# Performance work log

Measured on AMD Instinct MI355X. Metric: run time of the kernel, lower is better.

## Reference

```python
import jax, jax.numpy as jnp
import numpy as np

WS = 800      # window size
HEADS = 3
DH = 24       # dim_head
LOWRANK_W = 30
NEG_SLOPE = 0.01  # LeakyReLU default
LN_EPS = 1e-5


def _layernorm(x, g, b):
    m = jnp.mean(x, axis=-1, keepdims=True)
    v = jnp.var(x, axis=-1, keepdims=True)
    return (x - m) * jax.lax.rsqrt(v + LN_EPS) * g + b


def setup_inputs() -> dict:
    key = jax.random.key(0)
    ks = jax.random.split(key, 20)
    B, CIN, H, W = 2, 5, 160, 160
    D = 48
    INNER = HEADS * DH  # 72
    f32 = jnp.float32

    def n(k, shape, s=0.05):
        return jax.random.normal(k, shape, f32) * s

    return {
        "x": jax.random.normal(ks[0], (B, CIN, H, W), f32),
        # Embedding: Conv2d(5, 48, 3, pad=1) + PReLU
        "conv_w": n(ks[1], (D, CIN, 3, 3), 0.1),
        "conv_b": jnp.zeros((D,), f32),
        "prelu_a": jnp.array(0.25, f32),
        # attention PreNorm
        "ln1_g": jnp.ones((D,), f32),
        "ln1_b": jnp.zeros((D,), f32),
        # to_qkv: Linear(48, 216, bias=False)
        "w_qkv": n(ks[2], (3 * INNER, D)),
        # Linformer low-rank params E,F: [heads, dim_head, w]
        "E_mat": jax.random.normal(ks[3], (HEADS, DH, LOWRANK_W), f32),
        "F_mat": jax.random.normal(ks[4], (HEADS, DH, LOWRANK_W), f32),
        # lin1/lin2: Linear(w, dim_head)
        "w_e": n(ks[5], (DH, LOWRANK_W)),
        "b_e": jnp.zeros((DH,), f32),
        "w_f": n(ks[6], (DH, LOWRANK_W)),
        "b_f": jnp.zeros((DH,), f32),
        # to_out: Linear(72, 48)
        "w_out": n(ks[7], (D, INNER)),
        "b_out": jnp.zeros((D,), f32),
        # FF PreNorm + MLP (dim=48, hidden=48)
        "ln2_g": jnp.ones((D,), f32),
        "ln2_b": jnp.zeros((D,), f32),
        "ff_w1": n(ks[8], (D, D)),
        "ff_b1": jnp.zeros((D,), f32),
        "ff_w2": n(ks[9], (D, D)),
        "ff_b2": jnp.zeros((D,), f32),
        # final lin1: Linear(48, 96)
        "w_fin": n(ks[10], (2 * D, D)),
        "b_fin": jnp.zeros((2 * D,), f32),
    }


def reference(x, conv_w, conv_b, prelu_a, ln1_g, ln1_b, w_qkv, E_mat, F_mat,
              w_e, b_e, w_f, b_f, w_out, b_out, ln2_g, ln2_b,
              ff_w1, ff_b1, ff_w2, ff_b2, w_fin, b_fin):
    B, _, H, W = x.shape
    # Embedding: conv3x3 same + PReLU
    E = jax.lax.conv_general_dilated(
        x, conv_w, (1, 1), ((1, 1), (1, 1)),
        dimension_numbers=("NCHW", "OIHW", "NCHW")) + conv_b[None, :, None, None]
    E = jnp.maximum(E, 0) + prelu_a * jnp.minimum(E, 0)
    D = E.shape[1]
    seq = E.reshape(B, D, H * W).transpose(0, 2, 1)  # [B, N, D]
    N = seq.shape[1]
    nw = N // WS

    # --- Residual(PreNorm(LinformerAttention_wind1)) ---
    xn = _layernorm(seq, ln1_g, ln1_b)
    xw = xn.reshape(B, nw, WS, D)                         # windows
    qkv = jnp.einsum("bwnc,oc->bwno", xw, w_qkv)          # [B,nw,WS,216]
    qkv = qkv.reshape(B, nw, WS, HEADS, 3 * DH).transpose(0, 1, 3, 2, 4)
    q, k, v = jnp.split(qkv, 3, axis=-1)                  # each [B,nw,h,WS,DH]
    # einsum 'b h n d, h d d -> b h n d' == scale by diagonal of lin(E/F)
    e_diag = jnp.einsum("hdw,dw->hd", E_mat, w_e) + b_e   # [h, DH]
    f_diag = jnp.einsum("hdw,dw->hd", F_mat, w_f) + b_f
    k = k * e_diag[None, None, :, None, :]
    v = v * f_diag[None, None, :, None, :]
    scale = DH ** -0.5
    dots = jnp.einsum("bwhid,bwhjd->bwhij", q, k) * scale  # [B,nw,h,WS,WS]
    attn = jax.nn.softmax(dots, axis=-1)
    ow = jnp.einsum("bwhij,bwhjd->bwhid", attn, v)
    ow = ow.transpose(0, 1, 3, 2, 4).reshape(B, N, HEADS * DH)
    att = jnp.einsum("bnf,of->bno", ow, w_out) + b_out
    seq = seq + att

    # --- Residual(PreNorm(FeedForward)) ---
    yn = _layernorm(seq, ln2_g, ln2_b)
    h = jnp.einsum("bnc,oc->bno", yn, ff_w1) + ff_b1
    h = jnp.where(h >= 0, h, NEG_SLOPE * h)
    h = jnp.einsum("bno,co->bnc", h, ff_w2) + ff_b2
    att1 = seq + h                                        # [B, N, D]

    hp = att1.transpose(0, 2, 1).reshape(B, D, H, W)
    Highpass1 = E * hp + E
    lin = jnp.einsum("bnc,oc->bno", att1, w_fin) + b_fin  # [B, N, 2D]
    return (Highpass1, lin)
```

## Files before the change

kernel.cpp:

```cpp
#include <hip/hip_runtime.h>
#include <hip/hip_bf16.h>

#define B_    2
#define CIN_  5
#define H_    160
#define W_    160
#define N_    25600
#define D_    48
#define NW_   32
#define WS_   800
#define HEADS_ 3
#define DH_   24
#define INNER_ 72
#define NWH_  192

typedef __bf16 bf16x8 __attribute__((ext_vector_type(8)));
typedef float  f32x4  __attribute__((ext_vector_type(4)));

#define MFMA(a,b,c) __builtin_amdgcn_mfma_f32_16x16x32_bf16((a),(b),(c),0,0,0)

__device__ __forceinline__ float fast_exp2(float x) {
#if __has_builtin(__builtin_amdgcn_exp2f)
    return __builtin_amdgcn_exp2f(x);
#else
    return exp2f(x);
#endif
}

__device__ __forceinline__ unsigned pack_bf16(float lo, float hi) {
    __bf16 l = (__bf16)lo, h = (__bf16)hi;
    unsigned short ul = __builtin_bit_cast(unsigned short, l);
    unsigned short uh = __builtin_bit_cast(unsigned short, h);
    return ((unsigned)uh << 16) | (unsigned)ul;
}

__global__ __launch_bounds__(256) void k_wprep(const float* __restrict__ wqkv,
                                               const float* __restrict__ w_out,
                                               const float* __restrict__ fw1,
                                               const float* __restrict__ fw2,
                                               const float* __restrict__ wfin,
                                               const float* __restrict__ cw,
                                               const float* __restrict__ Em,
                                               const float* __restrict__ Fm,
                                               const float* __restrict__ we,
                                               const float* __restrict__ be,
                                               const float* __restrict__ wf,
                                               const float* __restrict__ bf,
                                               float* __restrict__ diag,
                                               __bf16* __restrict__ wqB,
                                               __bf16* __restrict__ woB,
                                               __bf16* __restrict__ f1B,
                                               __bf16* __restrict__ f2B,
                                               __bf16* __restrict__ wfB,
                                               __bf16* __restrict__ wcB) {
    if (blockIdx.x == 0 && threadIdx.x < 72) {
        int tt = threadIdx.x;
        int h = tt / 24, d = tt % 24;
        float se = be[d], sf = bf[d];
        for (int w = 0; w < 30; ++w) {
            se += Em[(h*24+d)*30 + w] * we[d*30 + w];
            sf += Fm[(h*24+d)*30 + w] * wf[d*30 + w];
        }
        diag[tt]      = se;
        diag[72 + tt] = sf;
    }
    int t = blockIdx.x*256 + threadIdx.x, stride = gridDim.x*256;
    for (int i = t; i < 288*64; i += stride) {
        int grow = i>>6, c = i&63;
        int gg = grow>>5, q = grow&31, tt = q>>4, sp = q&15, d = tt*16+sp;
        int part = gg/3, head = gg%3;
        wqB[i] = (d<24 && c<48) ? (__bf16)wqkv[(head*72 + part*24 + d)*48 + c] : (__bf16)0.f;
    }
    for (int i = t; i < 48*96;  i += stride) {
        int o = i/96, p = i%96;
        int h = p>>5, q = p&31, j = q&1, sp = q>>1, d = j*16+sp;
        woB[i] = (d<24) ? (__bf16)w_out[o*72 + h*24 + d] : (__bf16)0.f;
    }
    for (int i = t; i < 48*64;  i += stride) { int o=i>>6, c=i&63; f1B[i] = (c<48)? (__bf16)fw1[o*48+c] : (__bf16)0.f; }
    for (int i = t; i < 48*64;  i += stride) { int o=i>>6, c=i&63; f2B[i] = (c<48)? (__bf16)fw2[o*48+c] : (__bf16)0.f; }
    for (int i = t; i < 96*64;  i += stride) { int o=i>>6, c=i&63; wfB[i] = (c<48)? (__bf16)wfin[o*48+c] : (__bf16)0.f; }
    for (int i = t; i < 48*64;  i += stride) { int o=i>>6, c=i&63; wcB[i] = (c<45)? (__bf16)cw[o*45+c] : (__bf16)0.f; }
}

__global__ __launch_bounds__(256) void k_cqkv(const float* __restrict__ x,
                                              const __bf16* __restrict__ wcB,
                                              const float* __restrict__ cb,
                                              const float* __restrict__ pa,
                                              const __bf16* __restrict__ wqB,
                                              const float* __restrict__ g1,
                                              const float* __restrict__ b1,
                                              const float* __restrict__ diag,
                                              float* __restrict__ seqT,
                                              __bf16* __restrict__ Qbf,
                                              __bf16* __restrict__ Kbf,
                                              __bf16* __restrict__ Vt) {
    __shared__ float Lx[CIN_][4][W_];
    __shared__ __bf16 xfer[64*64];
    int t = threadIdx.x;
    int blk = blockIdx.x;
    int b = blk / 400;
    int n0 = (blk % 400) * 64;
    int y0 = n0 / W_;

    for (int i = t; i < CIN_*4*W_; i += 256) {
        int ic = i / (4*W_), rem = i % (4*W_), yy = rem / W_, col = rem % W_;
        int yr = y0 - 1 + yy;
        float v = 0.f;
        if (yr >= 0 && yr < H_)
            v = x[((size_t)(b*CIN_ + ic)*H_ + yr)*W_ + col];
        Lx[ic][yy][col] = v;
    }
    __syncthreads();

    int wv = t >> 6, lane = t & 63, g = lane>>4, s = lane&15;
    char* xb = (char*)xfer;

    {
        int rloc0 = wv * 16;
        bf16x8 ac[2];
        {
            int row = rloc0 + s;
            int n  = n0 + row;
            int y  = n / W_, xx = n % W_;
            int dy = y - y0;
            #pragma unroll
            for (int kc = 0; kc < 2; ++kc) {
                int kbase = kc*32 + g*8;
                #pragma unroll
                for (int j = 0; j < 8; ++j) {
                    int k = kbase + j;
                    int ic = k / 9, rem = k % 9, ky = rem / 3, kx = rem % 3;
                    int xc = xx + kx - 1;
                    float v = 0.f;
                    if ((kc == 0 || k < 45) && xc >= 0 && xc < W_)
                        v = Lx[ic][dy + ky][xc];
                    ac[kc][j] = (__bf16)v;
                }
            }
        }
        const bf16x8* WC4 = (const bf16x8*)wcB;
        float a = pa[0];
        float cbv[3], g1v[3], b1v[3];
        #pragma unroll
        for (int n = 0; n < 3; ++n) {
            cbv[n] = cb[n*16+s]; g1v[n] = g1[n*16+s]; b1v[n] = b1[n*16+s];
        }
        float xr[3][4];
        #pragma unroll
        for (int n = 0; n < 3; ++n) {
            bf16x8 wb0 = WC4[(n*16+s)*8 + g];
            bf16x8 wb1 = WC4[(n*16+s)*8 + 4 + g];
            f32x4 c = {0.f,0.f,0.f,0.f};
            c = MFMA(ac[0], wb0, c);
            c = MFMA(ac[1], wb1, c);
            #pragma unroll
            for (int r = 0; r < 4; ++r) {
                float vv = c[r] + cbv[n];
                vv = vv >= 0.f ? vv : a * vv;
                xr[n][r] = vv;
            }
        }
        int grow0 = blk*64 + rloc0;
        #pragma unroll
        for (int n = 0; n < 3; ++n)
          #pragma unroll
          for (int r = 0; r < 4; ++r)
            seqT[(size_t)(grow0 + g*4 + r)*48 + n*16 + s] = xr[n][r];

        #pragma unroll
        for (int r = 0; r < 4; ++r) {
            float sm = xr[0][r] + xr[1][r] + xr[2][r];
            float sq = xr[0][r]*xr[0][r] + xr[1][r]*xr[1][r] + xr[2][r]*xr[2][r];
            #pragma unroll
            for (int msk = 1; msk < 16; msk <<= 1) { sm += __shfl_xor(sm, msk); sq += __shfl_xor(sq, msk); }
            float mean = sm * (1.f/48.f);
            float var  = sq * (1.f/48.f) - mean*mean;
            float rs   = rsqrtf(var + 1e-5f);
            int row = rloc0 + g*4 + r;
            int sw  = ((g*4+r)&7) << 4;
            #pragma unroll
            for (int n = 0; n < 3; ++n) {
                float yn = (xr[n][r] - mean) * rs * g1v[n] + b1v[n];
                *(__bf16*)(xb + ((row*128 + (n*16+s)*2) ^ sw)) = (__bf16)yn;
            }
            *(__bf16*)(xb + ((row*128 + (48+s)*2) ^ sw)) = (__bf16)0.f;
        }
    }
    __syncthreads();

    int rh = wv & 1, gh = wv >> 1;
    int growQ = blk*64 + rh*32;
    int nrem = growQ % N_;
    int w = nrem / WS_, i0 = nrem % WS_;
    size_t headbase = (size_t)((b*NW_ + w)*HEADS_);

    bf16x8 af[2][2];
    #pragma unroll
    for (int m = 0; m < 2; ++m)
      #pragma unroll
      for (int kc = 0; kc < 2; ++kc) {
        int row = rh*32 + m*16 + s;
        af[m][kc] = *(const bf16x8*)(xb + ((row*128 + kc*64 + g*16) ^ ((s&7)<<4)));
      }

    const bf16x8* WQ4 = (const bf16x8*)wqB;
    const float SCALE = 0.2944889919f;

    float dke[3], dko[3], dve[3], dvo[3];
    #pragma unroll
    for (int h = 0; h < 3; ++h) {
        dke[h] = diag[h*24 + s];
        dko[h] = (s < 8) ? diag[h*24 + 16 + s] : 0.f;
        dve[h] = diag[72 + h*24 + s];
        dvo[h] = (s < 8) ? diag[72 + h*24 + 16 + s] : 0.f;
    }

    unsigned* Qd = (unsigned*)Qbf;
    unsigned* Kd = (unsigned*)Kbf;

    int gg0 = gh ? 5 : 0, gg1 = gh ? 9 : 5;
    for (int gg = gg0; gg < gg1; ++gg) {
        int part = gg / 3, head = gg % 3;
        bf16x8 we0 = WQ4[(gg*32 +      s)*8 +     g];
        bf16x8 we1 = WQ4[(gg*32 +      s)*8 + 4 + g];
        bf16x8 wo0 = WQ4[(gg*32 + 16 + s)*8 +     g];
        bf16x8 wo1 = WQ4[(gg*32 + 16 + s)*8 + 4 + g];
        f32x4 ce[2], co[2];
        #pragma unroll
        for (int m = 0; m < 2; ++m) {
            f32x4 c = {0.f,0.f,0.f,0.f};
            c = MFMA(af[m][0], we0, c); c = MFMA(af[m][1], we1, c);
            ce[m] = c;
            f32x4 d = {0.f,0.f,0.f,0.f};
            d = MFMA(af[m][0], wo0, d); d = MFMA(af[m][1], wo1, d);
            co[m] = d;
        }
        size_t rbase = (headbase + head)*WS_ + i0;
        if (part == 0) {
            #pragma unroll
            for (int m = 0; m < 2; ++m)
              #pragma unroll
              for (int r = 0; r < 4; ++r)
                Qd[(rbase + m*16 + g*4 + r)*16 + s] =
                    pack_bf16(ce[m][r]*SCALE, co[m][r]*SCALE);
        } else if (part == 1) {
            #pragma unroll
            for (int m = 0; m < 2; ++m)
              #pragma unroll
              for (int r = 0; r < 4; ++r) {
                int p5 = 16*(g&1) + 8*m + 4*(g>>1) + r;
                Kd[(rbase + p5)*16 + s] =
                    pack_bf16(ce[m][r]*dke[head], co[m][r]*dko[head]);
              }
        } else {
            size_t vbase = (headbase + head)*((size_t)32*WS_) + i0;
            #pragma unroll
            for (int m = 0; m < 2; ++m)
              #pragma unroll
              for (int r = 0; r < 4; ++r) {
                int row = m*16 + g*4 + r;
                Vt[vbase + (size_t)s*WS_ + row] = (__bf16)(ce[m][r]*dve[head]);
                if (s < 8)
                    Vt[vbase + (size_t)(16+s)*WS_ + row] = (__bf16)(co[m][r]*dvo[head]);
              }
        }
    }
    if (gh == 1) {
        unsigned* Vd = (unsigned*)Vt;
        #pragma unroll
        for (int it = 0; it < 6; ++it) {
            int idx = it*64 + lane;
            int h = idx >> 7, rem = idx & 127;
            int dd = 24 + (rem >> 4), cp = rem & 15;
            size_t ubase = (((headbase + h)*((size_t)32*WS_) + (size_t)dd*WS_ + i0) >> 1);
            Vd[ubase + cp] = (dd == 24) ? 0x3F803F80u : 0u;
        }
    }
}

__global__ __launch_bounds__(256, 4) void k_attn(const __bf16* __restrict__ Qbf,
                                                 const __bf16* __restrict__ Kbf,
                                                 const __bf16* __restrict__ Vt,
                                                 __bf16* __restrict__ OW) {
    __shared__ float red[2][5][2][4][64];
    int t = threadIdx.x;
    int wv = t >> 6, lane = t & 63;
    int g = lane >> 4, s = lane & 15;
    int half = wv & 1, tsk = wv >> 1;
    int blk = blockIdx.x;
    int v = (blk & 7) * 120 + (blk >> 3);
    int task = v * 2 + tsk;
    int wh = task / 10, qt = task % 10;
    int q0 = qt * 80;

    const bf16x8* Qp = (const bf16x8*)(Qbf + ((size_t)wh*WS_ + q0)*32);
    const bf16x8* Kp = (const bf16x8*)(Kbf + (size_t)wh*WS_*32);
    const bf16x8* Vp = (const bf16x8*)(Vt  + (size_t)wh*32*WS_);

    bf16x8 qb[5];
    #pragma unroll
    for (int i = 0; i < 5; ++i) qb[i] = Qp[(i*16 + s)*4 + g];

    f32x4 o[5][2];
    #pragma unroll
    for (int i = 0; i < 5; ++i) {
        o[i][0] = (f32x4){0.f,0.f,0.f,0.f};
        o[i][1] = (f32x4){0.f,0.f,0.f,0.f};
    }

    int c0 = half ? 12 : 0;
    int c1 = half ? 25 : 12;

    bf16x8 ka0 = Kp[(c0*32 + s)*4 + g];
    bf16x8 ka1 = Kp[(c0*32 + 16 + s)*4 + g];
    bf16x8 vb0 = Vp[s*100 + c0*4 + g];
    bf16x8 vb1 = Vp[(16+s)*100 + c0*4 + g];

    for (int c = c0; c < c1; ++c) {
        int cn = (c + 1 < c1) ? c + 1 : c0;
        bf16x8 nk0 = Kp[(cn*32 + s)*4 + g];
        bf16x8 nk1 = Kp[(cn*32 + 16 + s)*4 + g];
        bf16x8 nv0 = Vp[s*100 + cn*4 + g];
        bf16x8 nv1 = Vp[(16+s)*100 + cn*4 + g];

        #pragma unroll
        for (int i = 0; i < 5; ++i) {
            f32x4 s0 = {0.f,0.f,0.f,0.f}, s1 = {0.f,0.f,0.f,0.f};
            s0 = MFMA(ka0, qb[i], s0);
            s1 = MFMA(ka1, qb[i], s1);
            bf16x8 pa;
            #pragma unroll
            for (int r = 0; r < 4; ++r) {
                pa[r]     = (__bf16)fast_exp2(s0[r]);
                pa[r + 4] = (__bf16)fast_exp2(s1[r]);
            }
            o[i][0] = MFMA(pa, vb0, o[i][0]);
            o[i][1] = MFMA(pa, vb1, o[i][1]);
        }
        ka0 = nk0; ka1 = nk1; vb0 = nv0; vb1 = nv1;
    }

    if (half) {
        #pragma unroll
        for (int i = 0; i < 5; ++i)
          #pragma unroll
          for (int j = 0; j < 2; ++j)
            #pragma unroll
            for (int r = 0; r < 4; ++r)
              red[tsk][i][j][r][lane] = o[i][j][r];
    }
    __syncthreads();
    if (!half) {
        #pragma unroll
        for (int i = 0; i < 5; ++i)
          #pragma unroll
          for (int j = 0; j < 2; ++j)
            #pragma unroll
            for (int r = 0; r < 4; ++r)
              o[i][j][r] += red[tsk][i][j][r][lane];

        int bw = wh / 3, h = wh % 3;
        int b = bw >> 5, w = bw & 31;
        unsigned* OWd = (unsigned*)OW;
        #pragma unroll
        for (int i = 0; i < 5; ++i) {
            #pragma unroll
            for (int r = 0; r < 4; ++r) {
                float den = __shfl(o[i][1][r], (lane & 48) + 8);
                float inv = 1.f / den;
                int n = w*WS_ + q0 + i*16 + g*4 + r;
                OWd[(size_t)(b*N_ + n)*48 + h*16 + s] =
                    pack_bf16(o[i][0][r]*inv, o[i][1][r]*inv);
            }
        }
    }
}

__global__ __launch_bounds__(256) void k_tail(const float* __restrict__ seqT,
                                              const __bf16* __restrict__ OW,
                                              const __bf16* __restrict__ woB,
                                              const float* __restrict__ b_out,
                                              const float* __restrict__ g2,
                                              const float* __restrict__ b2,
                                              const __bf16* __restrict__ f1B,
                                              const float* __restrict__ fb1,
                                              const __bf16* __restrict__ f2B,
                                              const float* __restrict__ fb2,
                                              const __bf16* __restrict__ wfB,
                                              const float* __restrict__ bfin,
                                              float* __restrict__ out1,
                                              float* __restrict__ out2) {
    __shared__ __bf16 xfer[4][1024];
    __shared__ float hp[4][16][49];
    int t = threadIdx.x, wv = t>>6, lane = t&63, g = lane>>4, s = lane&15;
    int row0 = (blockIdx.x*4 + wv) * 16;
    char* xb = (char*)&xfer[wv][0];

    int b = row0 / N_;
    int nbase = row0 % N_;

    const bf16x8* OW4 = (const bf16x8*)OW;
    const bf16x8* WO4 = (const bf16x8*)woB;
    const bf16x8* F14 = (const bf16x8*)f1B;
    const bf16x8* F24 = (const bf16x8*)f2B;
    const bf16x8* WF4 = (const bf16x8*)wfB;

    bf16x8 aow[3];
    #pragma unroll
    for (int kc = 0; kc < 3; ++kc)
        aow[kc] = OW4[(size_t)(row0 + s)*12 + kc*4 + g];

    f32x4 s2[3];
    #pragma unroll
    for (int n = 0; n < 3; ++n) {
        bf16x8 wb0 = WO4[(n*16+s)*12 + g];
        bf16x8 wb1 = WO4[(n*16+s)*12 + 4 + g];
        bf16x8 wb2 = WO4[(n*16+s)*12 + 8 + g];
        f32x4 c = {0.f,0.f,0.f,0.f};
        c = MFMA(aow[0], wb0, c);
        c = MFMA(aow[1], wb1, c);
        c = MFMA(aow[2], wb2, c);
        s2[n] = c;
    }
    float bov[3], g2v[3], b2v[3], f1bv[3], f2bv[3];
    #pragma unroll
    for (int n = 0; n < 3; ++n) {
        bov[n] = b_out[n*16+s]; g2v[n] = g2[n*16+s]; b2v[n] = b2[n*16+s];
        f1bv[n] = fb1[n*16+s];  f2bv[n] = fb2[n*16+s];
    }
    float sv[3][4];
    #pragma unroll
    for (int n = 0; n < 3; ++n)
      #pragma unroll
      for (int r = 0; r < 4; ++r) {
        sv[n][r] = seqT[(size_t)(row0 + g*4 + r)*48 + n*16 + s];
        s2[n][r] += sv[n][r] + bov[n];
      }

    #pragma unroll
    for (int r = 0; r < 4; ++r) {
        float sm = s2[0][r] + s2[1][r] + s2[2][r];
        float sq = s2[0][r]*s2[0][r] + s2[1][r]*s2[1][r] + s2[2][r]*s2[2][r];
        #pragma unroll
        for (int msk = 1; msk < 16; msk <<= 1) { sm += __shfl_xor(sm, msk); sq += __shfl_xor(sq, msk); }
        float mean = sm * (1.f/48.f);
        float var  = sq * (1.f/48.f) - mean*mean;
        float rs   = rsqrtf(var + 1e-5f);
        int row = g*4 + r;
        int sw  = (row&7) << 4;
        #pragma unroll
        for (int n = 0; n < 3; ++n) {
            float yn = (s2[n][r] - mean) * rs * g2v[n] + b2v[n];
            *(__bf16*)(xb + ((row*128 + (n*16+s)*2) ^ sw)) = (__bf16)yn;
        }
        *(__bf16*)(xb + ((row*128 + (48+s)*2) ^ sw)) = (__bf16)0.f;
    }

    bf16x8 af[2];
    f32x4 hh[3];

    #pragma unroll
    for (int kc = 0; kc < 2; ++kc)
        af[kc] = *(const bf16x8*)(xb + ((s*128 + kc*64 + g*16) ^ ((s&7)<<4)));
    #pragma unroll
    for (int n = 0; n < 3; ++n) {
        bf16x8 wb0 = F14[(n*16+s)*8 + g];
        bf16x8 wb1 = F14[(n*16+s)*8 + 4 + g];
        f32x4 c = {0.f,0.f,0.f,0.f};
        c = MFMA(af[0], wb0, c);
        c = MFMA(af[1], wb1, c);
        hh[n] = c;
    }
    #pragma unroll
    for (int r = 0; r < 4; ++r) {
        int row = g*4 + r;
        int sw  = (row&7) << 4;
        #pragma unroll
        for (int n = 0; n < 3; ++n) {
            float v = hh[n][r] + f1bv[n];
            v = v >= 0.f ? v : 0.01f*v;
            *(__bf16*)(xb + ((row*128 + (n*16+s)*2) ^ sw)) = (__bf16)v;
        }
        *(__bf16*)(xb + ((row*128 + (48+s)*2) ^ sw)) = (__bf16)0.f;
    }

    #pragma unroll
    for (int kc = 0; kc < 2; ++kc)
        af[kc] = *(const bf16x8*)(xb + ((s*128 + kc*64 + g*16) ^ ((s&7)<<4)));
    #pragma unroll
    for (int n = 0; n < 3; ++n) {
        bf16x8 wb0 = F24[(n*16+s)*8 + g];
        bf16x8 wb1 = F24[(n*16+s)*8 + 4 + g];
        f32x4 c = {0.f,0.f,0.f,0.f};
        c = MFMA(af[0], wb0, c);
        c = MFMA(af[1], wb1, c);
        hh[n] = c;
    }
    #pragma unroll
    for (int r = 0; r < 4; ++r) {
        int row = g*4 + r;
        int sw  = (row&7) << 4;
        #pragma unroll
        for (int n = 0; n < 3; ++n) {
            float a1v = s2[n][r] + hh[n][r] + f2bv[n];
            hp[wv][row][n*16+s] = sv[n][r] * (1.f + a1v);
            *(__bf16*)(xb + ((row*128 + (n*16+s)*2) ^ sw)) = (__bf16)a1v;
        }
        *(__bf16*)(xb + ((row*128 + (48+s)*2) ^ sw)) = (__bf16)0.f;
    }

    #pragma unroll
    for (int it = 0; it < 3; ++it) {
        int flat = it*256 + lane*4;
        int ch = flat >> 4, row = flat & 15;
        float4 v = { hp[wv][row][ch], hp[wv][row+1][ch],
                     hp[wv][row+2][ch], hp[wv][row+3][ch] };
        *(float4*)&out1[((size_t)b*D_ + ch)*N_ + nbase + row] = v;
    }

    #pragma unroll
    for (int kc = 0; kc < 2; ++kc)
        af[kc] = *(const bf16x8*)(xb + ((s*128 + kc*64 + g*16) ^ ((s&7)<<4)));
    #pragma unroll
    for (int n = 0; n < 6; ++n) {
        bf16x8 wb0 = WF4[(n*16+s)*8 + g];
        bf16x8 wb1 = WF4[(n*16+s)*8 + 4 + g];
        float bfv = bfin[n*16+s];
        f32x4 c = {0.f,0.f,0.f,0.f};
        c = MFMA(af[0], wb0, c);
        c = MFMA(af[1], wb1, c);
        #pragma unroll
        for (int r = 0; r < 4; ++r)
            out2[(size_t)(row0 + g*4 + r)*96 + n*16 + s] = c[r] + bfv;
    }
}

extern "C" void kernel_launch(void* const* d_in, const int* in_sizes, int n_in,
                              void* d_out, int out_size, void* d_ws, size_t ws_size,
                              hipStream_t stream) {
    const float* x      = (const float*)d_in[0];
    const float* conv_w = (const float*)d_in[1];
    const float* conv_b = (const float*)d_in[2];
    const float* prelu_a= (const float*)d_in[3];
    const float* ln1_g  = (const float*)d_in[4];
    const float* ln1_b  = (const float*)d_in[5];
    const float* w_qkv  = (const float*)d_in[6];
    const float* E_mat  = (const float*)d_in[7];
    const float* F_mat  = (const float*)d_in[8];
    const float* w_e    = (const float*)d_in[9];
    const float* b_e    = (const float*)d_in[10];
    const float* w_f    = (const float*)d_in[11];
    const float* b_f    = (const float*)d_in[12];
    const float* w_out  = (const float*)d_in[13];
    const float* b_out  = (const float*)d_in[14];
    const float* ln2_g  = (const float*)d_in[15];
    const float* ln2_b  = (const float*)d_in[16];
    const float* ff_w1  = (const float*)d_in[17];
    const float* ff_b1  = (const float*)d_in[18];
    const float* ff_w2  = (const float*)d_in[19];
    const float* ff_b2  = (const float*)d_in[20];
    const float* w_fin  = (const float*)d_in[21];
    const float* b_fin  = (const float*)d_in[22];

    float* ws = (float*)d_ws;
    float*  seqT = ws;
    float*  diag = seqT + (size_t)B_*N_*D_;
    __bf16* Qbf  = (__bf16*)(diag + 144);
    __bf16* Kbf  = Qbf + (size_t)NWH_*WS_*32;
    __bf16* Vt   = Kbf + (size_t)NWH_*WS_*32;
    __bf16* OW   = Vt + (size_t)NWH_*32*WS_;
    __bf16* wqB  = OW + (size_t)B_*N_*96;
    __bf16* woB  = wqB + 288*64;
    __bf16* f1B  = woB + 48*96;
    __bf16* f2B  = f1B + 48*64;
    __bf16* wfB  = f2B + 48*64;
    __bf16* wcB  = wfB + 96*64;

    float* out1 = (float*)d_out;
    float* out2 = out1 + (size_t)B_*D_*N_;

    k_wprep<<<32, 256, 0, stream>>>(w_qkv, w_out, ff_w1, ff_w2, w_fin, conv_w,
                                    E_mat, F_mat, w_e, b_e, w_f, b_f, diag,
                                    wqB, woB, f1B, f2B, wfB, wcB);
    k_cqkv<<<800, 256, 0, stream>>>(x, wcB, conv_b, prelu_a,
                                    wqB, ln1_g, ln1_b, diag, seqT, Qbf, Kbf, Vt);
    k_attn<<<960, 256, 0, stream>>>(Qbf, Kbf, Vt, OW);
    k_tail<<<800, 256, 0, stream>>>(seqT, OW, woB, b_out, ln2_g, ln2_b,
                                    f1B, ff_b1, f2B, ff_b2, wfB, b_fin,
                                    out1, out2);
}
```

Baseline: 84.53 us.

## Halve cqkv tile to 32 rows, shrink halo load, vectorize V stores, add setprio

The fused conv+LN+QKV kernel now handles 32 pixels per block instead of 64, doubling the grid to 1600 blocks. It loads only a small 3x34 input halo instead of four full image rows. Work is redistributed across four waves: two compute the conv, all split the nine QKV groups, and one writes the V padding rows early. QKV weights are prefetched before the barrier and V stores are packed into 64-bit writes. s_setprio is also wrapped around MFMA sections in the attention and tail kernels. Risks include only half the waves doing the conv stage, uneven group splits across waves, and the unknown effect of the priority hints.

```diff
diff --git a/kernel.cpp b/kernel.cpp
--- a/kernel.cpp
+++ b/kernel.cpp
@@ -94,48 +94,73 @@
                                               __bf16* __restrict__ Qbf,
                                               __bf16* __restrict__ Kbf,
                                               __bf16* __restrict__ Vt) {
-    __shared__ float Lx[CIN_][4][W_];
-    __shared__ __bf16 xfer[64*64];
+    __shared__ float Lx[CIN_][3][34];
+    __shared__ __bf16 xfer[32*64];
     int t = threadIdx.x;
     int blk = blockIdx.x;
-    int b = blk / 400;
-    int n0 = (blk % 400) * 64;
+    int b = blk / 800;
+    int n0 = (blk % 800) * 32;
     int y0 = n0 / W_;
-
-    for (int i = t; i < CIN_*4*W_; i += 256) {
-        int ic = i / (4*W_), rem = i % (4*W_), yy = rem / W_, col = rem % W_;
+    int x0 = n0 % W_;
+
+    for (int i = t; i < CIN_*3*34; i += 256) {
+        int ic = i / (3*34), rem = i % (3*34), yy = rem / 34, col = rem % 34;
         int yr = y0 - 1 + yy;
+        int xc = x0 - 1 + col;
         float v = 0.f;
-        if (yr >= 0 && yr < H_)
-            v = x[((size_t)(b*CIN_ + ic)*H_ + yr)*W_ + col];
+        if (yr >= 0 && yr < H_ && xc >= 0 && xc < W_)
+            v = x[((size_t)(b*CIN_ + ic)*H_ + yr)*W_ + xc];
         Lx[ic][yy][col] = v;
     }
-    __syncthreads();
 
     int wv = t >> 6, lane = t & 63, g = lane>>4, s = lane&15;
     char* xb = (char*)xfer;
 
-    {
+    int w = n0 / WS_, i0 = n0 % WS_;
+    size_t headbase = (size_t)((b*NW_ + w)*HEADS_);
+    const bf16x8* WQ4 = (const bf16x8*)wqB;
+    int gg0 = (wv < 3) ? wv*2 : 7;
+    int gg1 = (wv == 2) ? 7 : gg0 + 2;
+    bf16x8 we0 = WQ4[(gg0*32 +      s)*8 +     g];
+    bf16x8 we1 = WQ4[(gg0*32 +      s)*8 + 4 + g];
+    bf16x8 wo0 = WQ4[(gg0*32 + 16 + s)*8 +     g];
+    bf16x8 wo1 = WQ4[(gg0*32 + 16 + s)*8 + 4 + g];
+    float dke[3], dko[3], dve[3], dvo[3];
+    #pragma unroll
+    for (int h = 0; h < 3; ++h) {
+        dke[h] = diag[h*24 + s];
+        dko[h] = (s < 8) ? diag[h*24 + 16 + s] : 0.f;
+        dve[h] = diag[72 + h*24 + s];
+        dvo[h] = (s < 8) ? diag[72 + h*24 + 16 + s] : 0.f;
+    }
+    if (wv == 3) {
+        unsigned* Vd = (unsigned*)Vt;
+        #pragma unroll
+        for (int it = 0; it < 6; ++it) {
+            int idx = it*64 + lane;
+            int h = idx >> 7, rem = idx & 127;
+            int dd = 24 + (rem >> 4), cp = rem & 15;
+            size_t ubase = (((headbase + h)*((size_t)32*WS_) + (size_t)dd*WS_ + i0) >> 1);
+            Vd[ubase + cp] = (dd == 24) ? 0x3F803F80u : 0u;
+        }
+    }
+    __syncthreads();
+
+    if (wv < 2) {
         int rloc0 = wv * 16;
+        int rib = rloc0 + s;
         bf16x8 ac[2];
-        {
-            int row = rloc0 + s;
-            int n  = n0 + row;
-            int y  = n / W_, xx = n % W_;
-            int dy = y - y0;
-            #pragma unroll
-            for (int kc = 0; kc < 2; ++kc) {
-                int kbase = kc*32 + g*8;
-                #pragma unroll
-                for (int j = 0; j < 8; ++j) {
-                    int k = kbase + j;
-                    int ic = k / 9, rem = k % 9, ky = rem / 3, kx = rem % 3;
-                    int xc = xx + kx - 1;
-                    float v = 0.f;
-                    if ((kc == 0 || k < 45) && xc >= 0 && xc < W_)
-                        v = Lx[ic][dy + ky][xc];
-                    ac[kc][j] = (__bf16)v;
-                }
+        #pragma unroll
+        for (int kc = 0; kc < 2; ++kc) {
+            int kbase = kc*32 + g*8;
+            #pragma unroll
+            for (int j = 0; j < 8; ++j) {
+                int k = kbase + j;
+                int ic = k / 9, rem = k % 9, ky = rem / 3, kx = rem % 3;
+                float v = 0.f;
+                if (kc == 0 || k < 45)
+                    v = Lx[ic][ky][rib + kx];
+                ac[kc][j] = (__bf16)v;
             }
         }
         const bf16x8* WC4 = (const bf16x8*)wcB;
@@ -160,7 +185,7 @@
                 xr[n][r] = vv;
             }
         }
-        int grow0 = blk*64 + rloc0;
+        int grow0 = blk*32 + rloc0;
         #pragma unroll
         for (int n = 0; n < 3; ++n)
           #pragma unroll
@@ -188,44 +213,30 @@
     }
     __syncthreads();
 
-    int rh = wv & 1, gh = wv >> 1;
-    int growQ = blk*64 + rh*32;
-    int nrem = growQ % N_;
-    int w = nrem / WS_, i0 = nrem % WS_;
-    size_t headbase = (size_t)((b*NW_ + w)*HEADS_);
-
     bf16x8 af[2][2];
     #pragma unroll
     for (int m = 0; m < 2; ++m)
       #pragma unroll
       for (int kc = 0; kc < 2; ++kc) {
-        int row = rh*32 + m*16 + s;
+        int row = m*16 + s;
         af[m][kc] = *(const bf16x8*)(xb + ((row*128 + kc*64 + g*16) ^ ((s&7)<<4)));
       }
 
-    const bf16x8* WQ4 = (const bf16x8*)wqB;
     const float SCALE = 0.2944889919f;
-
-    float dke[3], dko[3], dve[3], dvo[3];
-    #pragma unroll
-    for (int h = 0; h < 3; ++h) {
-        dke[h] = diag[h*24 + s];
-        dko[h] = (s < 8) ? diag[h*24 + 16 + s] : 0.f;
-        dve[h] = diag[72 + h*24 + s];
-        dvo[h] = (s < 8) ? diag[72 + h*24 + 16 + s] : 0.f;
-    }
 
     unsigned* Qd = (unsigned*)Qbf;
     unsigned* Kd = (unsigned*)Kbf;
 
-    int gg0 = gh ? 5 : 0, gg1 = gh ? 9 : 5;
     for (int gg = gg0; gg < gg1; ++gg) {
         int part = gg / 3, head = gg % 3;
-        bf16x8 we0 = WQ4[(gg*32 +      s)*8 +     g];
-        bf16x8 we1 = WQ4[(gg*32 +      s)*8 + 4 + g];
-        bf16x8 wo0 = WQ4[(gg*32 + 16 + s)*8 +     g];
-        bf16x8 wo1 = WQ4[(gg*32 + 16 + s)*8 + 4 + g];
+        if (gg != gg0) {
+            we0 = WQ4[(gg*32 +      s)*8 +     g];
+            we1 = WQ4[(gg*32 +      s)*8 + 4 + g];
+            wo0 = WQ4[(gg*32 + 16 + s)*8 +     g];
+            wo1 = WQ4[(gg*32 + 16 + s)*8 + 4 + g];
+        }
         f32x4 ce[2], co[2];
+        __builtin_amdgcn_s_setprio(1);
         #pragma unroll
         for (int m = 0; m < 2; ++m) {
             f32x4 c = {0.f,0.f,0.f,0.f};
@@ -235,6 +246,7 @@
             d = MFMA(af[m][0], wo0, d); d = MFMA(af[m][1], wo1, d);
             co[m] = d;
         }
+        __builtin_amdgcn_s_setprio(0);
         size_t rbase = (headbase + head)*WS_ + i0;
         if (part == 0) {
             #pragma unroll
@@ -255,25 +267,18 @@
         } else {
             size_t vbase = (headbase + head)*((size_t)32*WS_) + i0;
             #pragma unroll
-            for (int m = 0; m < 2; ++m)
-              #pragma unroll
-              for (int r = 0; r < 4; ++r) {
-                int row = m*16 + g*4 + r;
-                Vt[vbase + (size_t)s*WS_ + row] = (__bf16)(ce[m][r]*dve[head]);
-                if (s < 8)
-                    Vt[vbase + (size_t)(16+s)*WS_ + row] = (__bf16)(co[m][r]*dvo[head]);
-              }
-        }
-    }
-    if (gh == 1) {
-        unsigned* Vd = (unsigned*)Vt;
-        #pragma unroll
-        for (int it = 0; it < 6; ++it) {
-            int idx = it*64 + lane;
-            int h = idx >> 7, rem = idx & 127;
-            int dd = 24 + (rem >> 4), cp = rem & 15;
-            size_t ubase = (((headbase + h)*((size_t)32*WS_) + (size_t)dd*WS_ + i0) >> 1);
-            Vd[ubase + cp] = (dd == 24) ? 0x3F803F80u : 0u;
+            for (int m = 0; m < 2; ++m) {
+                uint2 pe;
+                pe.x = pack_bf16(ce[m][0]*dve[head], ce[m][1]*dve[head]);
+                pe.y = pack_bf16(ce[m][2]*dve[head], ce[m][3]*dve[head]);
+                *(uint2*)&Vt[vbase + (size_t)s*WS_ + m*16 + g*4] = pe;
+                if (s < 8) {
+                    uint2 po;
+                    po.x = pack_bf16(co[m][0]*dvo[head], co[m][1]*dvo[head]);
+                    po.y = pack_bf16(co[m][2]*dvo[head], co[m][3]*dvo[head]);
+                    *(uint2*)&Vt[vbase + (size_t)(16+s)*WS_ + m*16 + g*4] = po;
+                }
+            }
         }
     }
 }
@@ -323,6 +328,7 @@
         bf16x8 nv0 = Vp[s*100 + cn*4 + g];
         bf16x8 nv1 = Vp[(16+s)*100 + cn*4 + g];
 
+        __builtin_amdgcn_s_setprio(1);
         #pragma unroll
         for (int i = 0; i < 5; ++i) {
             f32x4 s0 = {0.f,0.f,0.f,0.f}, s1 = {0.f,0.f,0.f,0.f};
@@ -337,6 +343,7 @@
             o[i][0] = MFMA(pa, vb0, o[i][0]);
             o[i][1] = MFMA(pa, vb1, o[i][1]);
         }
+        __builtin_amdgcn_s_setprio(0);
         ka0 = nk0; ka1 = nk1; vb0 = nv0; vb1 = nv1;
     }
 
@@ -411,6 +418,7 @@
         aow[kc] = OW4[(size_t)(row0 + s)*12 + kc*4 + g];
 
     f32x4 s2[3];
+    __builtin_amdgcn_s_setprio(1);
     #pragma unroll
     for (int n = 0; n < 3; ++n) {
         bf16x8 wb0 = WO4[(n*16+s)*12 + g];
@@ -422,6 +430,7 @@
         c = MFMA(aow[2], wb2, c);
         s2[n] = c;
     }
+    __builtin_amdgcn_s_setprio(0);
     float bov[3], g2v[3], b2v[3], f1bv[3], f2bv[3];
     #pragma unroll
     for (int n = 0; n < 3; ++n) {
@@ -462,6 +471,7 @@
     #pragma unroll
     for (int kc = 0; kc < 2; ++kc)
         af[kc] = *(const bf16x8*)(xb + ((s*128 + kc*64 + g*16) ^ ((s&7)<<4)));
+    __builtin_amdgcn_s_setprio(1);
     #pragma unroll
     for (int n = 0; n < 3; ++n) {
         bf16x8 wb0 = F14[(n*16+s)*8 + g];
@@ -471,6 +481,7 @@
         c = MFMA(af[1], wb1, c);
         hh[n] = c;
     }
+    __builtin_amdgcn_s_setprio(0);
     #pragma unroll
     for (int r = 0; r < 4; ++r) {
         int row = g*4 + r;
@@ -487,6 +498,7 @@
     #pragma unroll
     for (int kc = 0; kc < 2; ++kc)
         af[kc] = *(const bf16x8*)(xb + ((s*128 + kc*64 + g*16) ^ ((s&7)<<4)));
+    __builtin_amdgcn_s_setprio(1);
     #pragma unroll
     for (int n = 0; n < 3; ++n) {
         bf16x8 wb0 = F24[(n*16+s)*8 + g];
@@ -496,6 +508,7 @@
         c = MFMA(af[1], wb1, c);
         hh[n] = c;
     }
+    __builtin_amdgcn_s_setprio(0);
     #pragma unroll
     for (int r = 0; r < 4; ++r) {
         int row = g*4 + r;
@@ -526,9 +539,11 @@
         bf16x8 wb0 = WF4[(n*16+s)*8 + g];
         bf16x8 wb1 = WF4[(n*16+s)*8 + 4 + g];
         float bfv = bfin[n*16+s];
+        __builtin_amdgcn_s_setprio(1);
         f32x4 c = {0.f,0.f,0.f,0.f};
         c = MFMA(af[0], wb0, c);
         c = MFMA(af[1], wb1, c);
+        __builtin_amdgcn_s_setprio(0);
         #pragma unroll
         for (int r = 0; r < 4; ++r)
             out2[(size_t)(row0 + g*4 + r)*96 + n*16 + s] = c[r] + bfv;
@@ -582,8 +597,8 @@
     k_wprep<<<32, 256, 0, stream>>>(w_qkv, w_out, ff_w1, ff_w2, w_fin, conv_w,
                                     E_mat, F_mat, w_e, b_e, w_f, b_f, diag,
                                     wqB, woB, f1B, f2B, wfB, wcB);
-    k_cqkv<<<800, 256, 0, stream>>>(x, wcB, conv_b, prelu_a,
-                                    wqB, ln1_g, ln1_b, diag, seqT, Qbf, Kbf, Vt);
+    k_cqkv<<<1600, 256, 0, stream>>>(x, wcB, conv_b, prelu_a,
+                                     wqB, ln1_g, ln1_b, diag, seqT, Qbf, Kbf, Vt);
     k_attn<<<960, 256, 0, stream>>>(Qbf, Kbf, Vt, OW);
     k_tail<<<800, 256, 0, stream>>>(seqT, OW, woB, b_out, ln2_g, ln2_b,
                                     f1B, ff_b1, f2B, ff_b2, wfB, b_fin,
```

New measurement: 74.02 us. 12.4% less time.
